# Kernel tuning notes

Measured on AMD Instinct MI355X. Metric: run time of the kernel, lower is better.

The kernel has to match this reference:

```python
import jax, jax.numpy as jnp
import numpy as np

N, C, H, W = 4, 64, 64, 64
K = 3


def _unfold(x, k):
    """torch F.unfold with padding k//2: [n,c,h,w] -> [n, c*k*k, h*w].
    Feature ordering matches torch: index = c*k*k + i*k + j."""
    p = k // 2
    n, c, h, w = x.shape
    xp = jnp.pad(x, ((0, 0), (0, 0), (p, p), (p, p)))
    patches = jnp.stack(
        [xp[:, :, i:i + h, j:j + w] for i in range(k) for j in range(k)], axis=2
    )  # [n, c, k*k, h, w]
    return patches.reshape(n, c * k * k, h * w)


def _mask_vec(c, k):
    # causal patch mask from __init__: zero out center-and-right of middle row and all rows below
    m = np.ones((c, k, k), np.float32)
    m[:, k // 2, k // 2:] = 0
    m[:, k // 2 + 1:, :] = 0
    return jnp.asarray(m.reshape(1, c * k * k, 1))


def setup_inputs() -> dict:
    key = jax.random.key(0)
    k1, k2 = jax.random.split(key)
    y_hat = jax.random.normal(k1, (N, C, H, W), dtype=jnp.float32)
    y_prob = jax.random.uniform(k2, (N, 1, H, W), dtype=jnp.float32)
    return {"y_hat": y_hat, "y_prob": y_prob}


def reference(y_hat, y_prob):
    k = K
    n, c, h, w = y_hat.shape
    L = h * w
    mask = _mask_vec(c, k)

    u = _unfold(y_hat, k) * mask                              # [n, c*k*k, L]
    u = u / jnp.maximum(jnp.linalg.norm(u, axis=1, keepdims=True), 1e-12)
    R = jnp.einsum('nfl,nfm->nlm', u, u)                      # [n, L, L] cosine sims

    # eval path: keep strictly-upper triangle (causal: l < m)
    row = jnp.arange(L)[:, None]
    col = jnp.arange(L)[None, :]
    R = jnp.where(col > row, R, 0.0)

    R_star = jnp.max(R, axis=1)                               # [n, L]
    arg = jnp.argmax(R, axis=1).astype(jnp.int32)             # [n, L]

    y_unf = _unfold(y_hat, k)                                 # [n, c*k*k, L]
    ref_unfold = jnp.take_along_axis(y_unf, arg[:, None, :], axis=2)

    prob_unf = y_prob.reshape(n, -1, L)                       # 1x1 unfold
    U_unf = jnp.take_along_axis(prob_unf, arg[:, None, :], axis=2)

    S = R_star.reshape(n, 1, h, w)
    U = U_unf.reshape(n, -1, h, w)

    # eval-mode position-0 overrides
    S = S.at[:, :, 0, 0].set(1e-8)
    U = U.at[:, :, 0, 0].set(1e-8)
    ref_unfold = ref_unfold.at[:, :, 0].set(0.0)
    arg = arg.at[:, 0].set(-1)

    S = jnp.clip(S, 1e-8, 1.0)
    U = jnp.clip(U, 1e-8, 1.0)
    return S, U, ref_unfold, arg
```

## Files before the change

### kernel.cpp

```cpp
#include <hip/hip_runtime.h>
#include <stdint.h>

#define Nn 4
#define Cc 64
#define LL 4096
#define KK 256
#define TRI2 528

typedef _Float16 half8 __attribute__((ext_vector_type(8)));
typedef float f32x16 __attribute__((ext_vector_type(16)));
typedef float f32x4 __attribute__((ext_vector_type(4)));
typedef unsigned short ushort8v __attribute__((ext_vector_type(8)));

__device__ __forceinline__ unsigned f2ord(float f) {
    unsigned u = __float_as_uint(f);
    return u ^ ((u & 0x80000000u) ? 0xFFFFFFFFu : 0x80000000u);
}
__device__ __forceinline__ float ord2f(unsigned o) {
    unsigned u = (o & 0x80000000u) ? (o ^ 0x80000000u) : ~o;
    return __uint_as_float(u);
}
__device__ __forceinline__ unsigned short h2u(_Float16 h) {
    union { _Float16 f; unsigned short u; } x; x.f = h; return x.u;
}

__device__ __forceinline__ void pipe_barrier_vm4() {
    asm volatile("s_waitcnt lgkmcnt(0) vmcnt(4)" ::: "memory");
    __builtin_amdgcn_s_barrier();
    __builtin_amdgcn_sched_barrier(0);
}
__device__ __forceinline__ void pipe_barrier_vm0() {
    asm volatile("s_waitcnt lgkmcnt(0) vmcnt(0)" ::: "memory");
    __builtin_amdgcn_s_barrier();
    __builtin_amdgcn_sched_barrier(0);
}

__global__ __launch_bounds__(256) void build_v(const float* __restrict__ yhat,
                                               unsigned short* __restrict__ VhT,
                                               unsigned short* __restrict__ VlT,
                                               float* __restrict__ yhatT,
                                               unsigned long long* __restrict__ best) {
    int blk = blockIdx.x;
    int xcd = blk & 7;
    int n = xcd >> 1;
    int i64 = (blk >> 3) + (xcd & 1) * 128;
    int tid = threadIdx.x;
    if (tid < 16) best[(size_t)n * LL + i64 * 16 + tid] = 0ull;

    int cg = tid & 15;
    int l = i64 * 16 + (tid >> 4);
    int y = l >> 6, x = l & 63;
    const float* src = yhat + (size_t)n * (Cc * LL);

    float vals[16];
    float ctr[4];
    float sumsq = 0.f;
#pragma unroll
    for (int ci = 0; ci < 4; ++ci) {
        const float* p = src + (cg * 4 + ci) * LL;
        float t0 = (y > 0 && x > 0)  ? p[l - 65] : 0.f;
        float t1 = (y > 0)           ? p[l - 64] : 0.f;
        float t2 = (y > 0 && x < 63) ? p[l - 63] : 0.f;
        float t3 = (x > 0)           ? p[l - 1]  : 0.f;
        ctr[ci] = p[l];
        vals[ci * 4 + 0] = t0; vals[ci * 4 + 1] = t1;
        vals[ci * 4 + 2] = t2; vals[ci * 4 + 3] = t3;
        sumsq += t0 * t0 + t1 * t1 + t2 * t2 + t3 * t3;
    }
    sumsq += __shfl_xor(sumsq, 1, 64);
    sumsq += __shfl_xor(sumsq, 2, 64);
    sumsq += __shfl_xor(sumsq, 4, 64);
    sumsq += __shfl_xor(sumsq, 8, 64);
    float inv = 1.f / fmaxf(sqrtf(sumsq), 1e-12f);

    f32x4 cv; cv.x = ctr[0]; cv.y = ctr[1]; cv.z = ctr[2]; cv.w = ctr[3];
    *(f32x4*)(yhatT + ((size_t)n * LL + l) * 64 + cg * 4) = cv;

    size_t pk = ((((size_t)n * 128 + (l >> 5)) * 16 + cg) << 9) + (l & 31) * 8;
    unsigned short* dh = VhT + pk;
    unsigned short* dl = VlT + pk;
    ushort8v hA, hB, lA, lB;
#pragma unroll
    for (int kk = 0; kk < 16; ++kk) {
        float v = vals[kk] * inv;
        _Float16 h = (fabsf(v) < 6.1035e-5f) ? (_Float16)0 : (_Float16)v;
        _Float16 lo = (_Float16)((v - (float)h) * 2048.0f);
        unsigned short hu = h2u(h * (_Float16)2048.0f);
        unsigned short lu = h2u(lo);
        if (kk < 8) { hA[kk] = hu; lA[kk] = lu; }
        else        { hB[kk - 8] = hu; lB[kk - 8] = lu; }
    }
    *(ushort8v*)(dh)       = hA;
    *(ushort8v*)(dh + 256) = hB;
    *(ushort8v*)(dl)       = lA;
    *(ushort8v*)(dl + 256) = lB;
}

__global__ __launch_bounds__(256) void simmax(const unsigned short* __restrict__ Vh,
                                              const unsigned short* __restrict__ Vl,
                                              unsigned long long* __restrict__ best) {
    __shared__ __align__(16) unsigned short S[24576];

    int bx = blockIdx.x;
    int xcd = bx & 7, idx = bx >> 3;
    int n = xcd >> 1;
    int t = (xcd & 1) * 264 + idx;

    int J = (int)((sqrtf(32.f * (float)t + 4.f) - 2.f) * 0.0625f);
    while (8 * (J + 1) * (J + 1) + 2 * (J + 1) <= t) ++J;
    while (8 * J * J + 2 * J > t) --J;
    int r = t - (8 * J * J + 2 * J);
    int i, j;
    if (r < 16 * J) {
        int I = r >> 4, inner = r & 15;
        i = 4 * I + (inner & 3);
        j = 4 * J + (inner >> 2);
    } else {
        int rr = r - 16 * J;
        int dj = (rr >= 6) ? 3 : (rr >= 3) ? 2 : (rr >= 1) ? 1 : 0;
        int di = rr - ((dj * (dj + 1)) >> 1);
        i = 4 * J + di;
        j = 4 * J + dj;
    }
    int l0 = i * 128, m0 = j * 128;

    int tid = threadIdx.x;
    int w = tid >> 6, lane = tid & 63;
    int r5 = lane & 31, h5 = lane >> 5;
    int rw = (w & 1) * 64;
    int cw = (w >> 1) * 64;
    bool skip = (i == j) && (rw == 64) && (cw == 0);

    const unsigned short* VhB = Vh + (size_t)n * (LL * KK);
    const unsigned short* VlB = Vl + (size_t)n * (LL * KK);

    int aRow0 = l0 >> 5;
    int bRow0 = m0 >> 5;

    const unsigned short* gsrc[4];
    int lslot[4];
#pragma unroll
    for (int q = 0; q < 4; ++q) {
        int cidx = w * 4 + q;
        int side = cidx >> 3, rb = (cidx >> 1) & 3, lo = cidx & 1;
        int rowblk = (side ? bRow0 : aRow0) + rb;
        gsrc[q] = (lo ? VlB : VhB) + ((size_t)(rowblk * 16) << 9) + lane * 8;
        lslot[q] = cidx * 512;
    }

    int arb = (w & 1) * 2;
    int brb = (w >> 1) * 2;

    f32x16 acc[2][2];
#pragma unroll
    for (int r2 = 0; r2 < 2; ++r2)
#pragma unroll
        for (int c = 0; c < 2; ++c) acc[r2][c] = (f32x16)0.f;

#define GLDS(KQ, BN)                                                              \
    do {                                                                          \
        _Pragma("unroll")                                                         \
        for (int q = 0; q < 4; ++q)                                               \
            __builtin_amdgcn_global_load_lds(                                     \
                (const __attribute__((address_space(1))) void*)(gsrc[q] + (size_t)(KQ) * 512), \
                (__attribute__((address_space(3))) void*)(S + (BN) * 8192 + lslot[q]), 16, 0, 0); \
    } while (0)

    GLDS(0, 0);
    GLDS(1, 1);

#pragma unroll
    for (int kt = 0; kt < 8; ++kt) {
        const int b0 = (2 * kt) % 3;
        const int b1 = (2 * kt + 1) % 3;

        half8 al[2][2], ah[2][2], bl[2][2], bh[2][2];

        pipe_barrier_vm4();
        if (kt < 7) GLDS(2 * kt + 2, (2 * kt + 2) % 3);
        if (!skip) {
#pragma unroll
            for (int r2 = 0; r2 < 2; ++r2) {
                al[r2][0] = *(const half8*)(S + b0 * 8192 + ((arb + r2) * 2 + 1) * 512 + lane * 8);
                bh[r2][0] = *(const half8*)(S + b0 * 8192 + (8 + (brb + r2) * 2) * 512 + lane * 8);
            }
#pragma unroll
            for (int r2 = 0; r2 < 2; ++r2) {
                ah[r2][0] = *(const half8*)(S + b0 * 8192 + ((arb + r2) * 2) * 512 + lane * 8);
                bl[r2][0] = *(const half8*)(S + b0 * 8192 + (9 + (brb + r2) * 2) * 512 + lane * 8);
            }
            __builtin_amdgcn_s_setprio(1);
#pragma unroll
            for (int r2 = 0; r2 < 2; ++r2)
#pragma unroll
                for (int c = 0; c < 2; ++c)
                    acc[r2][c] = __builtin_amdgcn_mfma_f32_32x32x16_f16(al[r2][0], bh[c][0], acc[r2][c], 0, 0, 0);
            __builtin_amdgcn_s_setprio(0);
        }

        if (kt < 7) pipe_barrier_vm4();
        else        pipe_barrier_vm0();
        if (kt < 7) GLDS(2 * kt + 3, (2 * kt + 3) % 3);

        if (!skip) {
#pragma unroll
            for (int r2 = 0; r2 < 2; ++r2) {
                al[r2][1] = *(const half8*)(S + b1 * 8192 + ((arb + r2) * 2 + 1) * 512 + lane * 8);
                bh[r2][1] = *(const half8*)(S + b1 * 8192 + (8 + (brb + r2) * 2) * 512 + lane * 8);
            }
#pragma unroll
            for (int r2 = 0; r2 < 2; ++r2) {
                ah[r2][1] = *(const half8*)(S + b1 * 8192 + ((arb + r2) * 2) * 512 + lane * 8);
                bl[r2][1] = *(const half8*)(S + b1 * 8192 + (9 + (brb + r2) * 2) * 512 + lane * 8);
            }
            __builtin_amdgcn_s_setprio(1);
#pragma unroll
            for (int r2 = 0; r2 < 2; ++r2)
#pragma unroll
                for (int c = 0; c < 2; ++c)
                    acc[r2][c] = __builtin_amdgcn_mfma_f32_32x32x16_f16(al[r2][1], bh[c][1], acc[r2][c], 0, 0, 0);
#pragma unroll
            for (int kc = 0; kc < 2; ++kc)
#pragma unroll
                for (int r2 = 0; r2 < 2; ++r2)
#pragma unroll
                    for (int c = 0; c < 2; ++c)
                        acc[r2][c] = __builtin_amdgcn_mfma_f32_32x32x16_f16(ah[r2][kc], bl[c][kc], acc[r2][c], 0, 0, 0);
#pragma unroll
            for (int kc = 0; kc < 2; ++kc)
#pragma unroll
                for (int r2 = 0; r2 < 2; ++r2)
#pragma unroll
                    for (int c = 0; c < 2; ++c)
                        acc[r2][c] = __builtin_amdgcn_mfma_f32_32x32x16_f16(ah[r2][kc], bh[c][kc], acc[r2][c], 0, 0, 0);
            __builtin_amdgcn_s_setprio(0);
        }
    }
#undef GLDS

    if (skip) return;
    unsigned long long* bb = best + (size_t)n * LL;
    const float s = 1.f / 4194304.f;
#pragma unroll
    for (int c = 0; c < 2; ++c) {
        int m = m0 + cw + c * 32 + r5;
        unsigned long long key = 0ull;
#pragma unroll
        for (int r2 = 0; r2 < 2; ++r2)
#pragma unroll
            for (int g = 0; g < 16; ++g) {
                int l = l0 + rw + r2 * 32 + (g & 3) + 8 * (g >> 2) + 4 * h5;
                if (l < m) {
                    float v = acc[r2][c][g] * s;
                    unsigned long long k2 =
                        ((unsigned long long)f2ord(v) << 32) |
                        (unsigned long long)(0xFFFFFFFFu - (unsigned)l);
                    key = (k2 > key) ? k2 : key;
                }
            }
        unsigned long long o = __shfl_xor(key, 32, 64);
        key = (o > key) ? o : key;
        if (h5 == 0 && key != 0ull) atomicMax(bb + m, key);
    }
}

__global__ __launch_bounds__(256) void writeout(const float* __restrict__ yhatT,
                                                const float* __restrict__ yprob,
                                                const unsigned long long* __restrict__ best,
                                                float* __restrict__ out) {
    __shared__ float P[576 * 17];

    int blk = blockIdx.x;
    int xcd = blk & 7;
    int n = xcd >> 1;
    int mb = (blk >> 3) + (xcd & 1) * 128;
    int m0 = mb * 16;
    int tid = threadIdx.x;
    int ml = tid >> 4;
    int cs = (tid & 15) * 4;
    int m = m0 + ml;

    unsigned long long key = best[(size_t)n * LL + m];
    unsigned l = 0xFFFFFFFFu - (unsigned)(key & 0xFFFFFFFFull);
    float val = ord2f((unsigned)(key >> 32));
    bool zero = (m == 0);
    if (zero) l = 0;
    int ly = (int)(l >> 6), lx = (int)(l & 63);

    float* Sout = out;
    float* Uout = out + 16384;
    float* Rout = out + 32768;
    float* Aout = out + 9469952;

    if (cs == 0) {
        float S = zero ? 1e-8f : fminf(fmaxf(val, 1e-8f), 1.0f);
        float U = zero ? 1e-8f : fminf(fmaxf(yprob[(size_t)n * LL + l], 1e-8f), 1.0f);
        Sout[(size_t)n * LL + m] = S;
        Uout[(size_t)n * LL + m] = U;
        Aout[(size_t)n * LL + m] = zero ? -1.0f : (float)l;
    }

    const float* T = yhatT + ((size_t)n * LL) * 64;
#pragma unroll
    for (int i = 0; i < 3; ++i) {
        int yy = ly + i - 1;
        bool rok = (!zero) && (yy >= 0) && (yy < 64);
#pragma unroll
        for (int jj = 0; jj < 3; ++jj) {
            int xx = lx + jj - 1;
            f32x4 v; v.x = 0.f; v.y = 0.f; v.z = 0.f; v.w = 0.f;
            if (rok && xx >= 0 && xx < 64)
                v = *(const f32x4*)(T + ((size_t)(yy * 64 + xx)) * 64 + cs);
            int ij = i * 3 + jj;
            P[((cs + 0) * 9 + ij) * 17 + ml] = v.x;
            P[((cs + 1) * 9 + ij) * 17 + ml] = v.y;
            P[((cs + 2) * 9 + ij) * 17 + ml] = v.z;
            P[((cs + 3) * 9 + ij) * 17 + ml] = v.w;
        }
    }
    __syncthreads();

    float* R = Rout + (size_t)n * (576 * LL) + m0;
    int fl = tid >> 4;
    int mm2 = tid & 15;
#pragma unroll 1
    for (int it2 = 0; it2 < 36; ++it2) {
        int f = it2 * 16 + fl;
        float v = P[f * 17 + mm2];
        __builtin_nontemporal_store(v, R + (size_t)f * LL + mm2);
    }
}

extern "C" void kernel_launch(void* const* d_in, const int* in_sizes, int n_in,
                              void* d_out, int out_size, void* d_ws, size_t ws_size,
                              hipStream_t stream) {
    const float* yhat  = (const float*)d_in[0];
    const float* yprob = (const float*)d_in[1];
    float* out = (float*)d_out;

    unsigned short* VhT = (unsigned short*)d_ws;
    unsigned short* VlT = (unsigned short*)((char*)d_ws + 8388608);
    unsigned long long* best =
        (unsigned long long*)((char*)d_ws + 16777216);
    float* yhatT = (float*)((char*)d_ws + 16908288);

    build_v<<<1024, 256, 0, stream>>>(yhat, VhT, VlT, yhatT, best);
    simmax<<<Nn * TRI2, 256, 0, stream>>>(VhT, VlT, best);
    writeout<<<1024, 256, 0, stream>>>(yhatT, yprob, best, out);
}
```

Baseline: 151.5 us.

## Shrink simmax LDS to double buffer and raise occupancy to 4 blocks

```diff
diff --git a/kernel.cpp b/kernel.cpp
--- a/kernel.cpp
+++ b/kernel.cpp
@@ -24,12 +24,7 @@
     union { _Float16 f; unsigned short u; } x; x.f = h; return x.u;
 }
 
-__device__ __forceinline__ void pipe_barrier_vm4() {
-    asm volatile("s_waitcnt lgkmcnt(0) vmcnt(4)" ::: "memory");
-    __builtin_amdgcn_s_barrier();
-    __builtin_amdgcn_sched_barrier(0);
-}
-__device__ __forceinline__ void pipe_barrier_vm0() {
+__device__ __forceinline__ void pipe_barrier() {
     asm volatile("s_waitcnt lgkmcnt(0) vmcnt(0)" ::: "memory");
     __builtin_amdgcn_s_barrier();
     __builtin_amdgcn_sched_barrier(0);
@@ -96,10 +91,10 @@
     *(ushort8v*)(dl + 256) = lB;
 }
 
-__global__ __launch_bounds__(256) void simmax(const unsigned short* __restrict__ Vh,
-                                              const unsigned short* __restrict__ Vl,
-                                              unsigned long long* __restrict__ best) {
-    __shared__ __align__(16) unsigned short S[24576];
+__global__ __launch_bounds__(256, 4) void simmax(const unsigned short* __restrict__ Vh,
+                                                 const unsigned short* __restrict__ Vl,
+                                                 unsigned long long* __restrict__ best) {
+    __shared__ __align__(16) unsigned short S[16384];
 
     int bx = blockIdx.x;
     int xcd = bx & 7, idx = bx >> 3;
@@ -125,7 +120,8 @@
     int l0 = i * 128, m0 = j * 128;
 
     int tid = threadIdx.x;
-    int w = tid >> 6, lane = tid & 63;
+    int w = __builtin_amdgcn_readfirstlane(tid >> 6);
+    int lane = tid & 63;
     int r5 = lane & 31, h5 = lane >> 5;
     int rw = (w & 1) * 64;
     int cw = (w >> 1) * 64;
@@ -167,72 +163,74 @@
     } while (0)
 
     GLDS(0, 0);
-    GLDS(1, 1);
 
 #pragma unroll
     for (int kt = 0; kt < 8; ++kt) {
-        const int b0 = (2 * kt) % 3;
-        const int b1 = (2 * kt + 1) % 3;
-
-        half8 al[2][2], ah[2][2], bl[2][2], bh[2][2];
-
-        pipe_barrier_vm4();
-        if (kt < 7) GLDS(2 * kt + 2, (2 * kt + 2) % 3);
+        half8 ah0[2], bl0[2], bh0[2];
+
+        pipe_barrier();
+        GLDS(2 * kt + 1, 1);
         if (!skip) {
+            half8 al0[2];
 #pragma unroll
             for (int r2 = 0; r2 < 2; ++r2) {
-                al[r2][0] = *(const half8*)(S + b0 * 8192 + ((arb + r2) * 2 + 1) * 512 + lane * 8);
-                bh[r2][0] = *(const half8*)(S + b0 * 8192 + (8 + (brb + r2) * 2) * 512 + lane * 8);
+                al0[r2] = *(const half8*)(S + ((arb + r2) * 2 + 1) * 512 + lane * 8);
+                bh0[r2] = *(const half8*)(S + (8 + (brb + r2) * 2) * 512 + lane * 8);
             }
 #pragma unroll
             for (int r2 = 0; r2 < 2; ++r2) {
-                ah[r2][0] = *(const half8*)(S + b0 * 8192 + ((arb + r2) * 2) * 512 + lane * 8);
-                bl[r2][0] = *(const half8*)(S + b0 * 8192 + (9 + (brb + r2) * 2) * 512 + lane * 8);
+                ah0[r2] = *(const half8*)(S + ((arb + r2) * 2) * 512 + lane * 8);
+                bl0[r2] = *(const half8*)(S + (9 + (brb + r2) * 2) * 512 + lane * 8);
             }
             __builtin_amdgcn_s_setprio(1);
 #pragma unroll
             for (int r2 = 0; r2 < 2; ++r2)
 #pragma unroll
                 for (int c = 0; c < 2; ++c)
-                    acc[r2][c] = __builtin_amdgcn_mfma_f32_32x32x16_f16(al[r2][0], bh[c][0], acc[r2][c], 0, 0, 0);
+                    acc[r2][c] = __builtin_amdgcn_mfma_f32_32x32x16_f16(al0[r2], bh0[c], acc[r2][c], 0, 0, 0);
             __builtin_amdgcn_s_setprio(0);
         }
 
-        if (kt < 7) pipe_barrier_vm4();
-        else        pipe_barrier_vm0();
-        if (kt < 7) GLDS(2 * kt + 3, (2 * kt + 3) % 3);
-
+        pipe_barrier();
+        if (kt < 7) GLDS(2 * kt + 2, 0);
         if (!skip) {
+            half8 al1[2], ah1[2], bl1[2], bh1[2];
 #pragma unroll
             for (int r2 = 0; r2 < 2; ++r2) {
-                al[r2][1] = *(const half8*)(S + b1 * 8192 + ((arb + r2) * 2 + 1) * 512 + lane * 8);
-                bh[r2][1] = *(const half8*)(S + b1 * 8192 + (8 + (brb + r2) * 2) * 512 + lane * 8);
+                al1[r2] = *(const half8*)(S + 8192 + ((arb + r2) * 2 + 1) * 512 + lane * 8);
+                bh1[r2] = *(const half8*)(S + 8192 + (8 + (brb + r2) * 2) * 512 + lane * 8);
             }
 #pragma unroll
             for (int r2 = 0; r2 < 2; ++r2) {
-                ah[r2][1] = *(const half8*)(S + b1 * 8192 + ((arb + r2) * 2) * 512 + lane * 8);
-                bl[r2][1] = *(const half8*)(S + b1 * 8192 + (9 + (brb + r2) * 2) * 512 + lane * 8);
+                ah1[r2] = *(const half8*)(S + 8192 + ((arb + r2) * 2) * 512 + lane * 8);
+                bl1[r2] = *(const half8*)(S + 8192 + (9 + (brb + r2) * 2) * 512 + lane * 8);
             }
             __builtin_amdgcn_s_setprio(1);
 #pragma unroll
             for (int r2 = 0; r2 < 2; ++r2)
 #pragma unroll
                 for (int c = 0; c < 2; ++c)
-                    acc[r2][c] = __builtin_amdgcn_mfma_f32_32x32x16_f16(al[r2][1], bh[c][1], acc[r2][c], 0, 0, 0);
-#pragma unroll
-            for (int kc = 0; kc < 2; ++kc)
-#pragma unroll
-                for (int r2 = 0; r2 < 2; ++r2)
-#pragma unroll
-                    for (int c = 0; c < 2; ++c)
-                        acc[r2][c] = __builtin_amdgcn_mfma_f32_32x32x16_f16(ah[r2][kc], bl[c][kc], acc[r2][c], 0, 0, 0);
-#pragma unroll
-            for (int kc = 0; kc < 2; ++kc)
-#pragma unroll
-                for (int r2 = 0; r2 < 2; ++r2)
-#pragma unroll
-                    for (int c = 0; c < 2; ++c)
-                        acc[r2][c] = __builtin_amdgcn_mfma_f32_32x32x16_f16(ah[r2][kc], bh[c][kc], acc[r2][c], 0, 0, 0);
+                    acc[r2][c] = __builtin_amdgcn_mfma_f32_32x32x16_f16(al1[r2], bh1[c], acc[r2][c], 0, 0, 0);
+#pragma unroll
+            for (int r2 = 0; r2 < 2; ++r2)
+#pragma unroll
+                for (int c = 0; c < 2; ++c)
+                    acc[r2][c] = __builtin_amdgcn_mfma_f32_32x32x16_f16(ah0[r2], bl0[c], acc[r2][c], 0, 0, 0);
+#pragma unroll
+            for (int r2 = 0; r2 < 2; ++r2)
+#pragma unroll
+                for (int c = 0; c < 2; ++c)
+                    acc[r2][c] = __builtin_amdgcn_mfma_f32_32x32x16_f16(ah1[r2], bl1[c], acc[r2][c], 0, 0, 0);
+#pragma unroll
+            for (int r2 = 0; r2 < 2; ++r2)
+#pragma unroll
+                for (int c = 0; c < 2; ++c)
+                    acc[r2][c] = __builtin_amdgcn_mfma_f32_32x32x16_f16(ah0[r2], bh0[c], acc[r2][c], 0, 0, 0);
+#pragma unroll
+            for (int r2 = 0; r2 < 2; ++r2)
+#pragma unroll
+                for (int c = 0; c < 2; ++c)
+                    acc[r2][c] = __builtin_amdgcn_mfma_f32_32x32x16_f16(ah1[r2], bh1[c], acc[r2][c], 0, 0, 0);
             __builtin_amdgcn_s_setprio(0);
         }
     }
```

After: 157.1 us. 3.7% more time.

## Split simmax tile across eight waves with 64x32 per-wave sub-tiles

Applied to the files above, without the earlier changes.

```diff
diff --git a/kernel.cpp b/kernel.cpp
--- a/kernel.cpp
+++ b/kernel.cpp
@@ -24,8 +24,8 @@
     union { _Float16 f; unsigned short u; } x; x.f = h; return x.u;
 }
 
-__device__ __forceinline__ void pipe_barrier_vm4() {
-    asm volatile("s_waitcnt lgkmcnt(0) vmcnt(4)" ::: "memory");
+__device__ __forceinline__ void pipe_barrier_vm2() {
+    asm volatile("s_waitcnt lgkmcnt(0) vmcnt(2)" ::: "memory");
     __builtin_amdgcn_s_barrier();
     __builtin_amdgcn_sched_barrier(0);
 }
@@ -96,7 +96,7 @@
     *(ushort8v*)(dl + 256) = lB;
 }
 
-__global__ __launch_bounds__(256) void simmax(const unsigned short* __restrict__ Vh,
+__global__ __launch_bounds__(512) void simmax(const unsigned short* __restrict__ Vh,
                                               const unsigned short* __restrict__ Vl,
                                               unsigned long long* __restrict__ best) {
     __shared__ __align__(16) unsigned short S[24576];
@@ -125,11 +125,12 @@
     int l0 = i * 128, m0 = j * 128;
 
     int tid = threadIdx.x;
-    int w = tid >> 6, lane = tid & 63;
+    int w = __builtin_amdgcn_readfirstlane(tid >> 6);
+    int lane = tid & 63;
     int r5 = lane & 31, h5 = lane >> 5;
     int rw = (w & 1) * 64;
-    int cw = (w >> 1) * 64;
-    bool skip = (i == j) && (rw == 64) && (cw == 0);
+    int cw = (w >> 1) * 32;
+    bool skip = (i == j) && (rw == 64) && (cw < 64);
 
     const unsigned short* VhB = Vh + (size_t)n * (LL * KK);
     const unsigned short* VlB = Vl + (size_t)n * (LL * KK);
@@ -137,30 +138,29 @@
     int aRow0 = l0 >> 5;
     int bRow0 = m0 >> 5;
 
-    const unsigned short* gsrc[4];
-    int lslot[4];
-#pragma unroll
-    for (int q = 0; q < 4; ++q) {
-        int cidx = w * 4 + q;
+    int laneElem = lane * 8;
+    const unsigned short* gsrc[2];
+    int lslot[2];
+#pragma unroll
+    for (int q = 0; q < 2; ++q) {
+        int cidx = w * 2 + q;
         int side = cidx >> 3, rb = (cidx >> 1) & 3, lo = cidx & 1;
         int rowblk = (side ? bRow0 : aRow0) + rb;
-        gsrc[q] = (lo ? VlB : VhB) + ((size_t)(rowblk * 16) << 9) + lane * 8;
+        gsrc[q] = (lo ? VlB : VhB) + ((size_t)(rowblk * 16) << 9) + laneElem;
         lslot[q] = cidx * 512;
     }
 
     int arb = (w & 1) * 2;
-    int brb = (w >> 1) * 2;
-
-    f32x16 acc[2][2];
-#pragma unroll
-    for (int r2 = 0; r2 < 2; ++r2)
-#pragma unroll
-        for (int c = 0; c < 2; ++c) acc[r2][c] = (f32x16)0.f;
+    int brb = (w >> 1);
+
+    f32x16 acc[2];
+#pragma unroll
+    for (int r2 = 0; r2 < 2; ++r2) acc[r2] = (f32x16)0.f;
 
 #define GLDS(KQ, BN)                                                              \
     do {                                                                          \
         _Pragma("unroll")                                                         \
-        for (int q = 0; q < 4; ++q)                                               \
+        for (int q = 0; q < 2; ++q)                                               \
             __builtin_amdgcn_global_load_lds(                                     \
                 (const __attribute__((address_space(1))) void*)(gsrc[q] + (size_t)(KQ) * 512), \
                 (__attribute__((address_space(3))) void*)(S + (BN) * 8192 + lslot[q]), 16, 0, 0); \
@@ -174,65 +174,55 @@
         const int b0 = (2 * kt) % 3;
         const int b1 = (2 * kt + 1) % 3;
 
-        half8 al[2][2], ah[2][2], bl[2][2], bh[2][2];
-
-        pipe_barrier_vm4();
+        half8 ah0[2], bh0, bl0;
+
+        pipe_barrier_vm2();
         if (kt < 7) GLDS(2 * kt + 2, (2 * kt + 2) % 3);
         if (!skip) {
+            half8 al0[2];
 #pragma unroll
             for (int r2 = 0; r2 < 2; ++r2) {
-                al[r2][0] = *(const half8*)(S + b0 * 8192 + ((arb + r2) * 2 + 1) * 512 + lane * 8);
-                bh[r2][0] = *(const half8*)(S + b0 * 8192 + (8 + (brb + r2) * 2) * 512 + lane * 8);
+                al0[r2] = *(const half8*)(S + b0 * 8192 + ((arb + r2) * 2 + 1) * 512 + laneElem);
+                ah0[r2] = *(const half8*)(S + b0 * 8192 + ((arb + r2) * 2) * 512 + laneElem);
             }
-#pragma unroll
-            for (int r2 = 0; r2 < 2; ++r2) {
-                ah[r2][0] = *(const half8*)(S + b0 * 8192 + ((arb + r2) * 2) * 512 + lane * 8);
-                bl[r2][0] = *(const half8*)(S + b0 * 8192 + (9 + (brb + r2) * 2) * 512 + lane * 8);
-            }
+            bh0 = *(const half8*)(S + b0 * 8192 + (8 + brb * 2) * 512 + laneElem);
+            bl0 = *(const half8*)(S + b0 * 8192 + (9 + brb * 2) * 512 + laneElem);
             __builtin_amdgcn_s_setprio(1);
 #pragma unroll
             for (int r2 = 0; r2 < 2; ++r2)
-#pragma unroll
-                for (int c = 0; c < 2; ++c)
-                    acc[r2][c] = __builtin_amdgcn_mfma_f32_32x32x16_f16(al[r2][0], bh[c][0], acc[r2][c], 0, 0, 0);
+                acc[r2] = __builtin_amdgcn_mfma_f32_32x32x16_f16(al0[r2], bh0, acc[r2], 0, 0, 0);
             __builtin_amdgcn_s_setprio(0);
         }
 
-        if (kt < 7) pipe_barrier_vm4();
+        if (kt < 7) pipe_barrier_vm2();
         else        pipe_barrier_vm0();
         if (kt < 7) GLDS(2 * kt + 3, (2 * kt + 3) % 3);
 
         if (!skip) {
+            half8 al1[2], ah1[2], bh1, bl1;
 #pragma unroll
             for (int r2 = 0; r2 < 2; ++r2) {
-                al[r2][1] = *(const half8*)(S + b1 * 8192 + ((arb + r2) * 2 + 1) * 512 + lane * 8);
-                bh[r2][1] = *(const half8*)(S + b1 * 8192 + (8 + (brb + r2) * 2) * 512 + lane * 8);
+                al1[r2] = *(const half8*)(S + b1 * 8192 + ((arb + r2) * 2 + 1) * 512 + laneElem);
+                ah1[r2] = *(const half8*)(S + b1 * 8192 + ((arb + r2) * 2) * 512 + laneElem);
             }
-#pragma unroll
-            for (int r2 = 0; r2 < 2; ++r2) {
-                ah[r2][1] = *(const half8*)(S + b1 * 8192 + ((arb + r2) * 2) * 512 + lane * 8);
-                bl[r2][1] = *(const half8*)(S + b1 * 8192 + (9 + (brb + r2) * 2) * 512 + lane * 8);
-            }
+            bh1 = *(const half8*)(S + b1 * 8192 + (8 + brb * 2) * 512 + laneElem);
+            bl1 = *(const half8*)(S + b1 * 8192 + (9 + brb * 2) * 512 + laneElem);
             __builtin_amdgcn_s_setprio(1);
 #pragma unroll
             for (int r2 = 0; r2 < 2; ++r2)
-#pragma unroll
-                for (int c = 0; c < 2; ++c)
-                    acc[r2][c] = __builtin_amdgcn_mfma_f32_32x32x16_f16(al[r2][1], bh[c][1], acc[r2][c], 0, 0, 0);
-#pragma unroll
-            for (int kc = 0; kc < 2; ++kc)
-#pragma unroll
-                for (int r2 = 0; r2 < 2; ++r2)
-#pragma unroll
-                    for (int c = 0; c < 2; ++c)
-                        acc[r2][c] = __builtin_amdgcn_mfma_f32_32x32x16_f16(ah[r2][kc], bl[c][kc], acc[r2][c], 0, 0, 0);
-#pragma unroll
-            for (int kc = 0; kc < 2; ++kc)
-#pragma unroll
-                for (int r2 = 0; r2 < 2; ++r2)
-#pragma unroll
-                    for (int c = 0; c < 2; ++c)
-                        acc[r2][c] = __builtin_amdgcn_mfma_f32_32x32x16_f16(ah[r2][kc], bh[c][kc], acc[r2][c], 0, 0, 0);
+                acc[r2] = __builtin_amdgcn_mfma_f32_32x32x16_f16(al1[r2], bh1, acc[r2], 0, 0, 0);
+#pragma unroll
+            for (int r2 = 0; r2 < 2; ++r2)
+                acc[r2] = __builtin_amdgcn_mfma_f32_32x32x16_f16(ah0[r2], bl0, acc[r2], 0, 0, 0);
+#pragma unroll
+            for (int r2 = 0; r2 < 2; ++r2)
+                acc[r2] = __builtin_amdgcn_mfma_f32_32x32x16_f16(ah1[r2], bl1, acc[r2], 0, 0, 0);
+#pragma unroll
+            for (int r2 = 0; r2 < 2; ++r2)
+                acc[r2] = __builtin_amdgcn_mfma_f32_32x32x16_f16(ah0[r2], bh0, acc[r2], 0, 0, 0);
+#pragma unroll
+            for (int r2 = 0; r2 < 2; ++r2)
+                acc[r2] = __builtin_amdgcn_mfma_f32_32x32x16_f16(ah1[r2], bh1, acc[r2], 0, 0, 0);
             __builtin_amdgcn_s_setprio(0);
         }
     }
@@ -241,9 +231,8 @@
     if (skip) return;
     unsigned long long* bb = best + (size_t)n * LL;
     const float s = 1.f / 4194304.f;
-#pragma unroll
-    for (int c = 0; c < 2; ++c) {
-        int m = m0 + cw + c * 32 + r5;
+    {
+        int m = m0 + cw + r5;
         unsigned long long key = 0ull;
 #pragma unroll
         for (int r2 = 0; r2 < 2; ++r2)
@@ -251,7 +240,7 @@
             for (int g = 0; g < 16; ++g) {
                 int l = l0 + rw + r2 * 32 + (g & 3) + 8 * (g >> 2) + 4 * h5;
                 if (l < m) {
-                    float v = acc[r2][c][g] * s;
+                    float v = acc[r2][g] * s;
                     unsigned long long k2 =
                         ((unsigned long long)f2ord(v) << 32) |
                         (unsigned long long)(0xFFFFFFFFu - (unsigned)l);
@@ -345,6 +334,6 @@
     float* yhatT = (float*)((char*)d_ws + 16908288);
 
     build_v<<<1024, 256, 0, stream>>>(yhat, VhT, VlT, yhatT, best);
-    simmax<<<Nn * TRI2, 256, 0, stream>>>(VhT, VlT, best);
+    simmax<<<Nn * TRI2, 512, 0, stream>>>(VhT, VlT, best);
     writeout<<<1024, 256, 0, stream>>>(yhatT, yprob, best, out);
 }
```

Measured after the change: 150.4 us. Within noise of the previous version (-0.7%).

## Gather unfold directly from yhat planes in writeout, drop transposed copy

Applied to the files above, without the earlier changes.

```diff
diff --git a/kernel.cpp b/kernel.cpp
--- a/kernel.cpp
+++ b/kernel.cpp
@@ -9,7 +9,7 @@
 
 typedef _Float16 half8 __attribute__((ext_vector_type(8)));
 typedef float f32x16 __attribute__((ext_vector_type(16)));
-typedef float f32x4 __attribute__((ext_vector_type(4)));
+typedef float f4a __attribute__((ext_vector_type(4), aligned(4)));
 typedef unsigned short ushort8v __attribute__((ext_vector_type(8)));
 
 __device__ __forceinline__ unsigned f2ord(float f) {
@@ -38,7 +38,6 @@
 __global__ __launch_bounds__(256) void build_v(const float* __restrict__ yhat,
                                                unsigned short* __restrict__ VhT,
                                                unsigned short* __restrict__ VlT,
-                                               float* __restrict__ yhatT,
                                                unsigned long long* __restrict__ best) {
     int blk = blockIdx.x;
     int xcd = blk & 7;
@@ -53,7 +52,6 @@
     const float* src = yhat + (size_t)n * (Cc * LL);
 
     float vals[16];
-    float ctr[4];
     float sumsq = 0.f;
 #pragma unroll
     for (int ci = 0; ci < 4; ++ci) {
@@ -62,7 +60,6 @@
         float t1 = (y > 0)           ? p[l - 64] : 0.f;
         float t2 = (y > 0 && x < 63) ? p[l - 63] : 0.f;
         float t3 = (x > 0)           ? p[l - 1]  : 0.f;
-        ctr[ci] = p[l];
         vals[ci * 4 + 0] = t0; vals[ci * 4 + 1] = t1;
         vals[ci * 4 + 2] = t2; vals[ci * 4 + 3] = t3;
         sumsq += t0 * t0 + t1 * t1 + t2 * t2 + t3 * t3;
@@ -72,9 +69,6 @@
     sumsq += __shfl_xor(sumsq, 4, 64);
     sumsq += __shfl_xor(sumsq, 8, 64);
     float inv = 1.f / fmaxf(sqrtf(sumsq), 1e-12f);
-
-    f32x4 cv; cv.x = ctr[0]; cv.y = ctr[1]; cv.z = ctr[2]; cv.w = ctr[3];
-    *(f32x4*)(yhatT + ((size_t)n * LL + l) * 64 + cg * 4) = cv;
 
     size_t pk = ((((size_t)n * 128 + (l >> 5)) * 16 + cg) << 9) + (l & 31) * 8;
     unsigned short* dh = VhT + pk;
@@ -264,21 +258,21 @@
     }
 }
 
-__global__ __launch_bounds__(256) void writeout(const float* __restrict__ yhatT,
+__global__ __launch_bounds__(256) void writeout(const float* __restrict__ yhat,
                                                 const float* __restrict__ yprob,
                                                 const unsigned long long* __restrict__ best,
                                                 float* __restrict__ out) {
-    __shared__ float P[576 * 17];
-
     int blk = blockIdx.x;
     int xcd = blk & 7;
     int n = xcd >> 1;
-    int mb = (blk >> 3) + (xcd & 1) * 128;
-    int m0 = mb * 16;
+    int idx = (blk >> 3) + (xcd & 1) * 512;
+    int mb = idx >> 4;
+    int fc = idx & 15;
     int tid = threadIdx.x;
-    int ml = tid >> 4;
-    int cs = (tid & 15) * 4;
-    int m = m0 + ml;
+    int mm = tid & 63;
+    int fs = tid >> 6;
+    int c = fc * 4 + fs;
+    int m = mb * 64 + mm;
 
     unsigned long long key = best[(size_t)n * LL + m];
     unsigned l = 0xFFFFFFFFu - (unsigned)(key & 0xFFFFFFFFull);
@@ -292,7 +286,7 @@
     float* Rout = out + 32768;
     float* Aout = out + 9469952;
 
-    if (cs == 0) {
+    if (fc == 0 && fs == 0) {
         float S = zero ? 1e-8f : fminf(fmaxf(val, 1e-8f), 1.0f);
         float U = zero ? 1e-8f : fminf(fmaxf(yprob[(size_t)n * LL + l], 1e-8f), 1.0f);
         Sout[(size_t)n * LL + m] = S;
@@ -300,34 +294,29 @@
         Aout[(size_t)n * LL + m] = zero ? -1.0f : (float)l;
     }
 
-    const float* T = yhatT + ((size_t)n * LL) * 64;
-#pragma unroll
-    for (int i = 0; i < 3; ++i) {
-        int yy = ly + i - 1;
-        bool rok = (!zero) && (yy >= 0) && (yy < 64);
-#pragma unroll
-        for (int jj = 0; jj < 3; ++jj) {
-            int xx = lx + jj - 1;
-            f32x4 v; v.x = 0.f; v.y = 0.f; v.z = 0.f; v.w = 0.f;
-            if (rok && xx >= 0 && xx < 64)
-                v = *(const f32x4*)(T + ((size_t)(yy * 64 + xx)) * 64 + cs);
-            int ij = i * 3 + jj;
-            P[((cs + 0) * 9 + ij) * 17 + ml] = v.x;
-            P[((cs + 1) * 9 + ij) * 17 + ml] = v.y;
-            P[((cs + 2) * 9 + ij) * 17 + ml] = v.z;
-            P[((cs + 3) * 9 + ij) * 17 + ml] = v.w;
+    const float* src = yhat + (size_t)n * (Cc * LL);
+    const float* plane = src + (size_t)c * LL;
+    float* dst = Rout + (size_t)n * (576 * LL) + m;
+    bool fast = (!zero) && (lx >= 1) && (lx <= 61);
+#pragma unroll
+    for (int r3 = 0; r3 < 3; ++r3) {
+        int yy = ly + r3 - 1;
+        bool rowok = (!zero) && (yy >= 0) && (yy < 64);
+        float t0 = 0.f, t1 = 0.f, t2 = 0.f;
+        if (rowok) {
+            if (fast) {
+                f4a v = *(const f4a*)(plane + yy * 64 + lx - 1);
+                t0 = v.x; t1 = v.y; t2 = v.z;
+            } else {
+                if (lx > 0)  t0 = plane[yy * 64 + lx - 1];
+                t1 = plane[yy * 64 + lx];
+                if (lx < 63) t2 = plane[yy * 64 + lx + 1];
+            }
         }
-    }
-    __syncthreads();
-
-    float* R = Rout + (size_t)n * (576 * LL) + m0;
-    int fl = tid >> 4;
-    int mm2 = tid & 15;
-#pragma unroll 1
-    for (int it2 = 0; it2 < 36; ++it2) {
-        int f = it2 * 16 + fl;
-        float v = P[f * 17 + mm2];
-        __builtin_nontemporal_store(v, R + (size_t)f * LL + mm2);
+        size_t f = (size_t)(c * 9 + r3 * 3) * LL;
+        __builtin_nontemporal_store(t0, dst + f);
+        __builtin_nontemporal_store(t1, dst + f + LL);
+        __builtin_nontemporal_store(t2, dst + f + 2 * (size_t)LL);
     }
 }
 
@@ -342,9 +331,8 @@
     unsigned short* VlT = (unsigned short*)((char*)d_ws + 8388608);
     unsigned long long* best =
         (unsigned long long*)((char*)d_ws + 16777216);
-    float* yhatT = (float*)((char*)d_ws + 16908288);
-
-    build_v<<<1024, 256, 0, stream>>>(yhat, VhT, VlT, yhatT, best);
+
+    build_v<<<1024, 256, 0, stream>>>(yhat, VhT, VlT, best);
     simmax<<<Nn * TRI2, 256, 0, stream>>>(VhT, VlT, best);
-    writeout<<<1024, 256, 0, stream>>>(yhatT, yprob, best, out);
-}
+    writeout<<<4096, 256, 0, stream>>>(yhat, yprob, best, out);
+}
```

Result: faster. 147.0 us (-2.9%).
